# Kernel tuning notes

Measured on AMD Instinct MI355X. Metric: run time of the kernel, lower is better.

Reference implementation:

```python
import jax, jax.numpy as jnp
import numpy as np

B, S, D = 2, 2048, 1024
H = 2048          # expert hidden size; up-proj width is 2*H (GLU)
E = 8             # num_experts
K = 2             # top_k


def setup_inputs() -> dict:
    key = jax.random.key(0)
    k1, k2, k3, k4, k5 = jax.random.split(key, 5)
    x = jax.random.normal(k1, (B, S, D), dtype=jnp.float32)
    expert_p = jax.random.uniform(k2, (B, S, K), dtype=jnp.float32)
    expert_idxs = jax.random.randint(k3, (B, S, K), 0, E)
    W1 = jax.random.normal(k4, (E, D, 2 * H), dtype=jnp.float32) * 0.02
    W2 = jax.random.normal(k5, (E, H, D), dtype=jnp.float32) * 0.02
    return {"x": x, "expert_p": expert_p, "expert_idxs": expert_idxs, "W1": W1, "W2": W2}


def reference(x, expert_p, expert_idxs, W1, W2):
    # x: [B, S, D]; expert_p/expert_idxs: [B, S, K]; W1: [E, D, 2H]; W2: [E, H, D]
    x_shape = x.shape
    d = x_shape[-1]
    k = expert_idxs.shape[-1]
    n_experts = W1.shape[0]
    xf = x.reshape(-1, d)                      # [T, D]
    T = xf.shape[0]
    e_flat = expert_idxs.reshape(-1)           # [P] token-major pair order, P = T*k
    xp = jnp.repeat(xf, k, axis=0)             # [P, D] matches e_flat ordering

    # Grouped up-projection: each (token, expert) pair hits its expert's W1.
    up = jnp.zeros((T * k, W1.shape[-1]), dtype=x.dtype)
    for e in range(n_experts):                 # fixed small loop over experts
        up = up + jnp.where((e_flat == e)[:, None], xp @ W1[e], 0)

    # Fused GLU: chunk(2), exact GELU (torch nn.GELU default), gate (g + 1).
    h, g = jnp.split(up, 2, axis=-1)           # [P, H] each
    a = jax.nn.gelu(h, approximate=False) * (g + 1)

    # Grouped down-projection.
    down = jnp.zeros((T * k, d), dtype=x.dtype)
    for e in range(n_experts):
        down = down + jnp.where((e_flat == e)[:, None], a @ W2[e], 0)

    # Gated scatter-combine over the top_k pairs of each token.
    gates = expert_p.reshape(T, k)             # [T, K]
    y = jnp.sum(down.reshape(T, k, d) * gates[..., None], axis=1)
    return y.reshape(*x_shape[:-1], d)
```

## Files before the change

kernel.cpp:

```cpp
#include <hip/hip_runtime.h>
#include <hip/hip_bf16.h>
#include <math.h>

#define TT 4096
#define PP 8192
#define DD 1024
#define HH 2048
#define EE 8
#define CC1 4096

typedef __attribute__((ext_vector_type(8))) short s16x8;
typedef __attribute__((ext_vector_type(4))) float f32x4;

#define W1T_OFF   0ull
#define W2T_OFF   (W1T_OFF + (size_t)EE*DD*CC1*2)
#define XB_OFF    (W2T_OFF + (size_t)EE*HH*DD*2)
#define ABUF_OFF  (XB_OFF  + (size_t)TT*DD*2)
#define DOWN_OFF  (ABUF_OFF + (size_t)PP*HH*2)
#define META_OFF  (DOWN_OFF + (size_t)2*PP*DD*2)
#define PAIR_OFF  (META_OFF + 2048)
#define POS_OFF   (PAIR_OFF + (size_t)PP*4)

#define VMCNT(N) asm volatile("s_waitcnt vmcnt(" #N ")" ::: "memory")
#define CFENCE() asm volatile("" ::: "memory")

__device__ __forceinline__ unsigned short f2bf(float f) {
  union { float f; unsigned u; } a; a.f = f;
  unsigned u = a.u;
  unsigned r = u + 0x7FFFu + ((u >> 16) & 1u);
  return (unsigned short)(r >> 16);
}

__device__ __forceinline__ float bf2f(unsigned short s) {
  union { unsigned u; float f; } a; a.u = ((unsigned)s) << 16;
  return a.f;
}

__device__ __forceinline__ void gload16(const void* g, void* l) {
  __builtin_amdgcn_global_load_lds(
      (const __attribute__((address_space(1))) void*)(uintptr_t)g,
      (__attribute__((address_space(3))) void*)(unsigned)(uintptr_t)l,
      16, 0, 0);
}

__device__ __forceinline__ void transpose_tile(const float* __restrict__ in,
                                               unsigned short* __restrict__ out,
                                               int R, int C, int bx, int by, int bz,
                                               float (*t)[65], int tid) {
  const size_t mbase = (size_t)bz * (size_t)R * (size_t)C;
  int c0 = bx * 64, r0 = by * 64;
#pragma unroll
  for (int i = 0; i < 4; ++i) {
    int ch = tid + i * 256;
    int row = ch >> 4, c4 = (ch & 15) * 4;
    float4 v = *reinterpret_cast<const float4*>(&in[mbase + (size_t)(r0 + row) * C + c0 + c4]);
    t[row][c4] = v.x; t[row][c4 + 1] = v.y; t[row][c4 + 2] = v.z; t[row][c4 + 3] = v.w;
  }
  __syncthreads();
#pragma unroll
  for (int i = 0; i < 4; ++i) {
    int ch = tid + i * 256;
    int c = ch >> 4, rb = (ch & 15) * 4;
    ushort4 o;
    o.x = f2bf(t[rb][c]); o.y = f2bf(t[rb + 1][c]);
    o.z = f2bf(t[rb + 2][c]); o.w = f2bf(t[rb + 3][c]);
    *reinterpret_cast<ushort4*>(&out[mbase + (size_t)(c0 + c) * R + r0 + rb]) = o;
  }
}

__global__ __launch_bounds__(256) void k_prep(
    const float* __restrict__ x, unsigned short* __restrict__ xb,
    const float* __restrict__ W1, unsigned short* __restrict__ w1t,
    const float* __restrict__ W2, unsigned short* __restrict__ w2t,
    const int* __restrict__ eidx, int* __restrict__ meta,
    int* __restrict__ plist, int* __restrict__ pos) {
  __shared__ float t[64][65];
  __shared__ int cnt[EE], off[EE + 1], cur[EE];
  const int b = blockIdx.x;
  const int tid = threadIdx.x;

  if (b == 0) {
    if (tid < EE) { cnt[tid] = 0; cur[tid] = 0; }
    __syncthreads();
    for (int p = tid; p < PP; p += blockDim.x) atomicAdd(&cnt[eidx[p]], 1);
    __syncthreads();
    if (tid == 0) {
      int s = 0;
      for (int e = 0; e < EE; ++e) { off[e] = s; s += cnt[e]; }
      off[EE] = s;
      int n256 = 0;
      for (int e = 0; e < EE; ++e)
        for (int r = 0; r < cnt[e]; r += 256) {
          meta[16 + 2*n256] = e; meta[17 + 2*n256] = off[e] + r; ++n256;
        }
      meta[0] = n256;
      for (int e = 0; e <= EE; ++e) meta[1 + e] = off[e];
    }
    __syncthreads();
    for (int p = tid; p < PP; p += blockDim.x) {
      int e = eidx[p];
      int q = off[e] + atomicAdd(&cur[e], 1);
      plist[q] = p;
      pos[p] = q;
    }
  } else if (b < 1 + 4096) {
    int i = (b - 1) * 256 + tid;
    float4 v = reinterpret_cast<const float4*>(x)[i];
    ushort4 o;
    o.x = f2bf(v.x); o.y = f2bf(v.y); o.z = f2bf(v.z); o.w = f2bf(v.w);
    reinterpret_cast<ushort4*>(xb)[i] = o;
  } else if (b < 1 + 4096 + 8192) {
    int flat = b - (1 + 4096);
    transpose_tile(W1, w1t, DD, CC1, flat & 63, (flat >> 6) & 15, flat >> 10, t, tid);
  } else {
    int flat = b - (1 + 4096 + 8192);
    transpose_tile(W2, w2t, HH, DD, flat & 15, (flat >> 4) & 31, flat >> 9, t, tid);
  }
}

__global__ __launch_bounds__(512) void k_gemm1(
    const unsigned short* __restrict__ xb,
    const unsigned short* __restrict__ w1t,
    const float* __restrict__ gates,
    const int* __restrict__ meta,
    const int* __restrict__ plist,
    unsigned short* __restrict__ abuf)
{
  const int nt = meta[0];
  const int tb = blockIdx.x;
  if (tb >= nt) return;
  const int e  = meta[16 + 2*tb];
  const int q0 = meta[17 + 2*tb];
  const int nrows = min(256, meta[2 + e] - q0);
  const int c0 = blockIdx.y * 64;

  __shared__ unsigned short As[3][256 * 64];
  __shared__ unsigned short Bs[3][128 * 64];

  const int tid = threadIdx.x;
  const int wave = tid >> 6, lane = tid & 63;
  const int l15 = lane & 15, l4 = lane >> 4;
  const int wr = wave >> 1, wc = wave & 1;

  const unsigned short* w1e = w1t + (size_t)e * CC1 * DD;

  const unsigned short* aga[4];
  const unsigned short* bga[2];
#pragma unroll
  for (int i = 0; i < 4; ++i) {
    int c = tid + i * 512;
    int row = c >> 3;
    int ko = ((c & 7) ^ (row & 7)) * 8;
    int r = row < nrows ? row : 0;
    int p = plist[q0 + r];
    aga[i] = xb + (size_t)(p >> 1) * DD + ko;
  }
#pragma unroll
  for (int i = 0; i < 2; ++i) {
    int c = tid + i * 512;
    int row = c >> 3;
    int ko = ((c & 7) ^ (row & 7)) * 8;
    int u = row & 63, wcq = row >> 6;
    int col = (u < 32) ? (c0 + wcq * 32 + u) : (HH + c0 + wcq * 32 + (u - 32));
    bga[i] = w1e + (size_t)col * DD + ko;
  }

  f32x4 acc[4][4];
#pragma unroll
  for (int a = 0; a < 4; ++a)
#pragma unroll
    for (int b = 0; b < 4; ++b) acc[a][b] = (f32x4)0.0f;

  auto stage = [&](int kk, unsigned short* pa, unsigned short* pb) {
#pragma unroll
    for (int i = 0; i < 4; ++i) gload16(aga[i] + kk, pa + (tid + i * 512) * 8);
#pragma unroll
    for (int i = 0; i < 2; ++i) gload16(bga[i] + kk, pb + (tid + i * 512) * 8);
  };

  auto compute_tile = [&](const unsigned short* sa, const unsigned short* sb) {
    const char* A8 = (const char*)sa;
    const char* B8 = (const char*)sb;
#pragma unroll
    for (int ks = 0; ks < 2; ++ks) {
      s16x8 af[4], bfr[4];
#pragma unroll
      for (int rf = 0; rf < 4; ++rf) {
        int row = wr * 64 + rf * 16 + l15;
        af[rf] = *(const s16x8*)(A8 + ((row * 128 + ks * 64 + l4 * 16) ^ ((row & 7) << 4)));
      }
#pragma unroll
      for (int cf = 0; cf < 4; ++cf) {
        int row = wc * 64 + cf * 16 + l15;
        bfr[cf] = *(const s16x8*)(B8 + ((row * 128 + ks * 64 + l4 * 16) ^ ((row & 7) << 4)));
      }
#pragma unroll
      for (int rf = 0; rf < 4; ++rf)
#pragma unroll
        for (int cf = 0; cf < 4; ++cf)
          acc[rf][cf] = __builtin_amdgcn_mfma_f32_16x16x32_bf16(af[rf], bfr[cf], acc[rf][cf], 0, 0, 0);
    }
  };

  stage(0, As[0], Bs[0]);
  stage(64, As[1], Bs[1]);
  VMCNT(6);
  __builtin_amdgcn_s_barrier();
  CFENCE();

#pragma unroll
  for (int kt = 0; kt < 14; ++kt) {
    stage((kt + 2) * 64, As[(kt + 2) % 3], Bs[(kt + 2) % 3]);
    compute_tile(As[kt % 3], Bs[kt % 3]);
    VMCNT(6);
    __builtin_amdgcn_s_barrier();
    CFENCE();
  }
  compute_tile(As[14 % 3], Bs[14 % 3]);
  VMCNT(0);
  __builtin_amdgcn_s_barrier();
  CFENCE();
  compute_tile(As[15 % 3], Bs[15 % 3]);

#pragma unroll
  for (int rf = 0; rf < 4; ++rf) {
#pragma unroll
    for (int i = 0; i < 4; ++i) {
      int r = wr * 64 + rf * 16 + l4 * 4 + i;
      if (r < nrows) {
        int q = q0 + r;
        float gt = gates[plist[q]];
        unsigned short* orow = abuf + (size_t)q * HH + c0 + wc * 32 + l15;
#pragma unroll
        for (int cf = 0; cf < 2; ++cf) {
          float hv = acc[rf][cf][i];
          float gv = acc[rf][cf + 2][i];
          float av = 0.5f * hv * (1.0f + erff(hv * 0.70710678118654752f)) * (gv + 1.0f) * gt;
          orow[cf * 16] = f2bf(av);
        }
      }
    }
  }
}

__global__ __launch_bounds__(512) void k_gemm2(
    const unsigned short* __restrict__ abuf,
    const unsigned short* __restrict__ w2t,
    const int* __restrict__ meta,
    unsigned short* __restrict__ down)
{
  const int nt = meta[0];
  const int tb = blockIdx.x;
  if (tb >= nt) return;
  const int e  = meta[16 + 2*tb];
  const int q0 = meta[17 + 2*tb];
  const int nrows = min(256, meta[2 + e] - q0);
  const int c0 = blockIdx.y * 128;
  const int kz = blockIdx.z * (HH / 2);

  __shared__ unsigned short As[3][256 * 64];
  __shared__ unsigned short Bs[3][128 * 64];

  const int tid = threadIdx.x;
  const int wave = tid >> 6, lane = tid & 63;
  const int l15 = lane & 15, l4 = lane >> 4;
  const int wr = wave >> 1, wc = wave & 1;

  const unsigned short* w2e = w2t + (size_t)e * DD * HH;

  const unsigned short* aga[4];
  const unsigned short* bga[2];
#pragma unroll
  for (int i = 0; i < 4; ++i) {
    int c = tid + i * 512;
    int row = c >> 3;
    int ko = ((c & 7) ^ (row & 7)) * 8;
    int r = row < nrows ? row : 0;
    aga[i] = abuf + (size_t)(q0 + r) * HH + kz + ko;
  }
#pragma unroll
  for (int i = 0; i < 2; ++i) {
    int c = tid + i * 512;
    int row = c >> 3;
    int ko = ((c & 7) ^ (row & 7)) * 8;
    bga[i] = w2e + (size_t)(c0 + row) * HH + kz + ko;
  }

  f32x4 acc[4][4];
#pragma unroll
  for (int a = 0; a < 4; ++a)
#pragma unroll
    for (int b = 0; b < 4; ++b) acc[a][b] = (f32x4)0.0f;

  auto stage = [&](int kk, unsigned short* pa, unsigned short* pb) {
#pragma unroll
    for (int i = 0; i < 4; ++i) gload16(aga[i] + kk, pa + (tid + i * 512) * 8);
#pragma unroll
    for (int i = 0; i < 2; ++i) gload16(bga[i] + kk, pb + (tid + i * 512) * 8);
  };

  auto compute_tile = [&](const unsigned short* sa, const unsigned short* sb) {
    const char* A8 = (const char*)sa;
    const char* B8 = (const char*)sb;
#pragma unroll
    for (int ks = 0; ks < 2; ++ks) {
      s16x8 af[4], bfr[4];
#pragma unroll
      for (int rf = 0; rf < 4; ++rf) {
        int row = wr * 64 + rf * 16 + l15;
        af[rf] = *(const s16x8*)(A8 + ((row * 128 + ks * 64 + l4 * 16) ^ ((row & 7) << 4)));
      }
#pragma unroll
      for (int cf = 0; cf < 4; ++cf) {
        int row = wc * 64 + cf * 16 + l15;
        bfr[cf] = *(const s16x8*)(B8 + ((row * 128 + ks * 64 + l4 * 16) ^ ((row & 7) << 4)));
      }
#pragma unroll
      for (int rf = 0; rf < 4; ++rf)
#pragma unroll
        for (int cf = 0; cf < 4; ++cf)
          acc[rf][cf] = __builtin_amdgcn_mfma_f32_16x16x32_bf16(af[rf], bfr[cf], acc[rf][cf], 0, 0, 0);
    }
  };

  stage(0, As[0], Bs[0]);
  stage(64, As[1], Bs[1]);
  VMCNT(6);
  __builtin_amdgcn_s_barrier();
  CFENCE();

#pragma unroll
  for (int kt = 0; kt < 14; ++kt) {
    stage((kt + 2) * 64, As[(kt + 2) % 3], Bs[(kt + 2) % 3]);
    compute_tile(As[kt % 3], Bs[kt % 3]);
    VMCNT(6);
    __builtin_amdgcn_s_barrier();
    CFENCE();
  }
  compute_tile(As[14 % 3], Bs[14 % 3]);
  VMCNT(0);
  __builtin_amdgcn_s_barrier();
  CFENCE();
  compute_tile(As[15 % 3], Bs[15 % 3]);

  unsigned short* dz = down + (size_t)blockIdx.z * PP * DD;
#pragma unroll
  for (int rf = 0; rf < 4; ++rf) {
#pragma unroll
    for (int i = 0; i < 4; ++i) {
      int r = wr * 64 + rf * 16 + l4 * 4 + i;
      if (r < nrows) {
        int q = q0 + r;
        unsigned short* orow = dz + (size_t)q * DD + c0 + wc * 64 + l15;
#pragma unroll
        for (int cf = 0; cf < 4; ++cf) orow[cf * 16] = f2bf(acc[rf][cf][i]);
      }
    }
  }
}

__global__ void k_combine(const unsigned short* __restrict__ down, const int* __restrict__ pos,
                          float* __restrict__ y) {
  int i = blockIdx.x * blockDim.x + threadIdx.x;
  if (i >= TT * DD / 8) return;
  int t = i >> 7;
  int c8 = (i & 127) * 8;
  int qa = pos[2 * t], qb = pos[2 * t + 1];
  const unsigned short* d0 = down;
  const unsigned short* d1 = down + (size_t)PP * DD;
  s16x8 va0 = *reinterpret_cast<const s16x8*>(d0 + (size_t)qa * DD + c8);
  s16x8 va1 = *reinterpret_cast<const s16x8*>(d1 + (size_t)qa * DD + c8);
  s16x8 vb0 = *reinterpret_cast<const s16x8*>(d0 + (size_t)qb * DD + c8);
  s16x8 vb1 = *reinterpret_cast<const s16x8*>(d1 + (size_t)qb * DD + c8);
  float o[8];
#pragma unroll
  for (int j = 0; j < 8; ++j)
    o[j] = bf2f((unsigned short)va0[j]) + bf2f((unsigned short)va1[j]) +
           bf2f((unsigned short)vb0[j]) + bf2f((unsigned short)vb1[j]);
  float4* yo = reinterpret_cast<float4*>(y + (size_t)t * DD + c8);
  yo[0] = (float4){o[0], o[1], o[2], o[3]};
  yo[1] = (float4){o[4], o[5], o[6], o[7]};
}

extern "C" void kernel_launch(void* const* d_in, const int* in_sizes, int n_in,
                              void* d_out, int out_size, void* d_ws, size_t ws_size,
                              hipStream_t stream) {
  const float* x  = (const float*)d_in[0];
  const float* ep = (const float*)d_in[1];
  const int*   ei = (const int*)d_in[2];
  const float* W1 = (const float*)d_in[3];
  const float* W2 = (const float*)d_in[4];
  float* y = (float*)d_out;
  char* ws = (char*)d_ws;

  unsigned short* w1t = (unsigned short*)(ws + W1T_OFF);
  unsigned short* w2t = (unsigned short*)(ws + W2T_OFF);
  unsigned short* xb  = (unsigned short*)(ws + XB_OFF);
  unsigned short* ab  = (unsigned short*)(ws + ABUF_OFF);
  unsigned short* down = (unsigned short*)(ws + DOWN_OFF);
  int* meta   = (int*)(ws + META_OFF);
  int* plist  = (int*)(ws + PAIR_OFF);
  int* pos    = (int*)(ws + POS_OFF);

  hipLaunchKernelGGL(k_prep, dim3(1 + 4096 + 8192 + 4096), dim3(256), 0, stream,
                     x, xb, W1, w1t, W2, w2t, ei, meta, plist, pos);
  hipLaunchKernelGGL(k_gemm1, dim3(40, 32), dim3(512), 0, stream,
                     xb, w1t, ep, meta, plist, ab);
  hipLaunchKernelGGL(k_gemm2, dim3(40, 8, 2), dim3(512), 0, stream,
                     ab, w2t, meta, down);
  hipLaunchKernelGGL(k_combine, dim3(TT * DD / 8 / 256), dim3(256), 0, stream,
                     down, pos, y);
}
```

Baseline: 244.4 us.

## Shrink down-proj tiles to 128 rows with 4-way split-K and alias partials buffer

The down-projection GEMM now uses 128-row expert tiles (a second tile list in meta), 256-thread blocks and a 4-way K split, so the grid grows from 640 to 2304 blocks. The aim is to fix wave-quantization imbalance on the CUs and raise occupancy. To keep LDS small, the triple-buffered async pipeline becomes a single buffer with a __syncthreads before and after each compute, which exposes load latency. The four bf16 partial sums reuse the W1 transposed region, which is no longer needed after gemm1. The combine kernel now reads and sums four partials, which adds memory traffic.

```diff
diff --git a/kernel.cpp b/kernel.cpp
--- a/kernel.cpp
+++ b/kernel.cpp
@@ -13,11 +13,11 @@
 typedef __attribute__((ext_vector_type(4))) float f32x4;
 
 #define W1T_OFF   0ull
+#define DOWN_OFF  W1T_OFF
 #define W2T_OFF   (W1T_OFF + (size_t)EE*DD*CC1*2)
 #define XB_OFF    (W2T_OFF + (size_t)EE*HH*DD*2)
 #define ABUF_OFF  (XB_OFF  + (size_t)TT*DD*2)
-#define DOWN_OFF  (ABUF_OFF + (size_t)PP*HH*2)
-#define META_OFF  (DOWN_OFF + (size_t)2*PP*DD*2)
+#define META_OFF  (ABUF_OFF + (size_t)PP*HH*2)
 #define PAIR_OFF  (META_OFF + 2048)
 #define POS_OFF   (PAIR_OFF + (size_t)PP*4)
 
@@ -94,6 +94,12 @@
           meta[16 + 2*n256] = e; meta[17 + 2*n256] = off[e] + r; ++n256;
         }
       meta[0] = n256;
+      int n128 = 0;
+      for (int e = 0; e < EE; ++e)
+        for (int r = 0; r < cnt[e]; r += 128) {
+          meta[128 + 2*n128] = e; meta[129 + 2*n128] = off[e] + r; ++n128;
+        }
+      meta[10] = n128;
       for (int e = 0; e <= EE; ++e) meta[1 + e] = off[e];
     }
     __syncthreads();
@@ -243,23 +249,23 @@
   }
 }
 
-__global__ __launch_bounds__(512) void k_gemm2(
+__global__ __launch_bounds__(256) void k_gemm2(
     const unsigned short* __restrict__ abuf,
     const unsigned short* __restrict__ w2t,
     const int* __restrict__ meta,
     unsigned short* __restrict__ down)
 {
-  const int nt = meta[0];
+  const int nt = meta[10];
   const int tb = blockIdx.x;
   if (tb >= nt) return;
-  const int e  = meta[16 + 2*tb];
-  const int q0 = meta[17 + 2*tb];
-  const int nrows = min(256, meta[2 + e] - q0);
+  const int e  = meta[128 + 2*tb];
+  const int q0 = meta[129 + 2*tb];
+  const int nrows = min(128, meta[2 + e] - q0);
   const int c0 = blockIdx.y * 128;
-  const int kz = blockIdx.z * (HH / 2);
-
-  __shared__ unsigned short As[3][256 * 64];
-  __shared__ unsigned short Bs[3][128 * 64];
+  const int kz = blockIdx.z * (HH / 4);
+
+  __shared__ unsigned short As[128 * 64];
+  __shared__ unsigned short Bs[128 * 64];
 
   const int tid = threadIdx.x;
   const int wave = tid >> 6, lane = tid & 63;
@@ -269,20 +275,14 @@
   const unsigned short* w2e = w2t + (size_t)e * DD * HH;
 
   const unsigned short* aga[4];
-  const unsigned short* bga[2];
+  const unsigned short* bga[4];
 #pragma unroll
   for (int i = 0; i < 4; ++i) {
-    int c = tid + i * 512;
+    int c = tid + i * 256;
     int row = c >> 3;
     int ko = ((c & 7) ^ (row & 7)) * 8;
     int r = row < nrows ? row : 0;
     aga[i] = abuf + (size_t)(q0 + r) * HH + kz + ko;
-  }
-#pragma unroll
-  for (int i = 0; i < 2; ++i) {
-    int c = tid + i * 512;
-    int row = c >> 3;
-    int ko = ((c & 7) ^ (row & 7)) * 8;
     bga[i] = w2e + (size_t)(c0 + row) * HH + kz + ko;
   }
 
@@ -292,16 +292,16 @@
 #pragma unroll
     for (int b = 0; b < 4; ++b) acc[a][b] = (f32x4)0.0f;
 
-  auto stage = [&](int kk, unsigned short* pa, unsigned short* pb) {
-#pragma unroll
-    for (int i = 0; i < 4; ++i) gload16(aga[i] + kk, pa + (tid + i * 512) * 8);
-#pragma unroll
-    for (int i = 0; i < 2; ++i) gload16(bga[i] + kk, pb + (tid + i * 512) * 8);
+  auto stage = [&](int kk) {
+#pragma unroll
+    for (int i = 0; i < 4; ++i) gload16(aga[i] + kk, As + (tid + i * 256) * 8);
+#pragma unroll
+    for (int i = 0; i < 4; ++i) gload16(bga[i] + kk, Bs + (tid + i * 256) * 8);
   };
 
-  auto compute_tile = [&](const unsigned short* sa, const unsigned short* sb) {
-    const char* A8 = (const char*)sa;
-    const char* B8 = (const char*)sb;
+  auto compute_tile = [&]() {
+    const char* A8 = (const char*)As;
+    const char* B8 = (const char*)Bs;
 #pragma unroll
     for (int ks = 0; ks < 2; ++ks) {
       s16x8 af[4], bfr[4];
@@ -323,25 +323,13 @@
     }
   };
 
-  stage(0, As[0], Bs[0]);
-  stage(64, As[1], Bs[1]);
-  VMCNT(6);
-  __builtin_amdgcn_s_barrier();
-  CFENCE();
-
-#pragma unroll
-  for (int kt = 0; kt < 14; ++kt) {
-    stage((kt + 2) * 64, As[(kt + 2) % 3], Bs[(kt + 2) % 3]);
-    compute_tile(As[kt % 3], Bs[kt % 3]);
-    VMCNT(6);
-    __builtin_amdgcn_s_barrier();
-    CFENCE();
-  }
-  compute_tile(As[14 % 3], Bs[14 % 3]);
-  VMCNT(0);
-  __builtin_amdgcn_s_barrier();
-  CFENCE();
-  compute_tile(As[15 % 3], Bs[15 % 3]);
+#pragma unroll
+  for (int kt = 0; kt < 8; ++kt) {
+    stage(kt * 64);
+    __syncthreads();
+    compute_tile();
+    if (kt < 7) __syncthreads();
+  }
 
   unsigned short* dz = down + (size_t)blockIdx.z * PP * DD;
 #pragma unroll
@@ -366,17 +354,18 @@
   int t = i >> 7;
   int c8 = (i & 127) * 8;
   int qa = pos[2 * t], qb = pos[2 * t + 1];
-  const unsigned short* d0 = down;
-  const unsigned short* d1 = down + (size_t)PP * DD;
-  s16x8 va0 = *reinterpret_cast<const s16x8*>(d0 + (size_t)qa * DD + c8);
-  s16x8 va1 = *reinterpret_cast<const s16x8*>(d1 + (size_t)qa * DD + c8);
-  s16x8 vb0 = *reinterpret_cast<const s16x8*>(d0 + (size_t)qb * DD + c8);
-  s16x8 vb1 = *reinterpret_cast<const s16x8*>(d1 + (size_t)qb * DD + c8);
   float o[8];
 #pragma unroll
-  for (int j = 0; j < 8; ++j)
-    o[j] = bf2f((unsigned short)va0[j]) + bf2f((unsigned short)va1[j]) +
-           bf2f((unsigned short)vb0[j]) + bf2f((unsigned short)vb1[j]);
+  for (int j = 0; j < 8; ++j) o[j] = 0.0f;
+#pragma unroll
+  for (int z = 0; z < 4; ++z) {
+    const unsigned short* dz = down + (size_t)z * PP * DD;
+    s16x8 va = *reinterpret_cast<const s16x8*>(dz + (size_t)qa * DD + c8);
+    s16x8 vb = *reinterpret_cast<const s16x8*>(dz + (size_t)qb * DD + c8);
+#pragma unroll
+    for (int j = 0; j < 8; ++j)
+      o[j] += bf2f((unsigned short)va[j]) + bf2f((unsigned short)vb[j]);
+  }
   float4* yo = reinterpret_cast<float4*>(y + (size_t)t * DD + c8);
   yo[0] = (float4){o[0], o[1], o[2], o[3]};
   yo[1] = (float4){o[4], o[5], o[6], o[7]};
@@ -406,7 +395,7 @@
                      x, xb, W1, w1t, W2, w2t, ei, meta, plist, pos);
   hipLaunchKernelGGL(k_gemm1, dim3(40, 32), dim3(512), 0, stream,
                      xb, w1t, ep, meta, plist, ab);
-  hipLaunchKernelGGL(k_gemm2, dim3(40, 8, 2), dim3(512), 0, stream,
+  hipLaunchKernelGGL(k_gemm2, dim3(72, 8, 4), dim3(256), 0, stream,
                      ab, w2t, meta, down);
   hipLaunchKernelGGL(k_combine, dim3(TT * DD / 8 / 256), dim3(256), 0, stream,
                      down, pos, y);
```

Result: slower. 257.9 us (+5.5%).
